# Performance work log

Measured on AMD Instinct MI355X. Metric: run time of the kernel, lower is better.

The kernel has to match this reference:

```python
import jax, jax.numpy as jnp
import numpy as np
from jax import lax

SIGMA = 0.03
ALPHA = 1.0
MASK_VALUE = -1e-8
SAMPLE_NUM = 131072  # static stand-in for the dynamic edge-pixel count


def _sobel_edges(images):
    # images: [n,3,h,w]; torch code uses only channel 0 when c==3
    kx = jnp.array([[-1., 0., 1.], [-2., 0., 2.], [-1., 0., 1.]], dtype=images.dtype).reshape(1, 1, 3, 3)
    ky = jnp.array([[1., 2., 1.], [0., 0., 0.], [-1., -2., -1.]], dtype=images.dtype).reshape(1, 1, 3, 3)
    x = images[:, :1]
    dn = ('NCHW', 'OIHW', 'NCHW')
    gx = lax.conv_general_dilated(x, kx, (1, 1), 'VALID', dimension_numbers=dn)
    gy = lax.conv_general_dilated(x, ky, (1, 1), 'VALID', dimension_numbers=dn)
    edges = jnp.sqrt(gx * gx + gy * gy)
    thetas = jnp.arctan2(gy, gx)
    pad = ((0, 0), (0, 0), (1, 1), (1, 1))
    return jnp.pad(edges, pad), jnp.pad(thetas, pad)


def _per_image_loss(inp, tgt, msk, edge, theta, ra, rd, rp, h, w):
    # all flat vectors of length P = h*w; ra:[S], rd:[4,S], rp:[2S]
    # --- edge-guided sampling ---
    emax = edge.max()
    emask = edge >= 0.1 * emax
    minlen = jnp.maximum(emask.sum(), 1)
    edge_idx = jnp.argsort(jnp.logical_not(emask), stable=True)  # edge pixels first
    anchor_pix = edge_idx[ra % minlen]
    theta_a = theta[anchor_pix]
    row_a = anchor_pix // w
    col_a = anchor_pix % w
    sign = jnp.array([-1., -1., 1., 1.], dtype=inp.dtype)[:, None]
    dist = (rd.astype(inp.dtype) + 2.0) * sign  # magnitudes in [2,31)
    col4 = jnp.clip(col_a[None, :] + jnp.round(dist * jnp.cos(theta_a)[None, :]).astype(jnp.int32), 0, w - 1)
    row4 = jnp.clip(row_a[None, :] + jnp.round(dist * jnp.sin(theta_a)[None, :]).astype(jnp.int32), 0, h - 1)
    pix = row4 * w + col4  # sub2ind, [4,S]
    A = jnp.concatenate([pix[0], pix[1], pix[2]])  # [3S]
    B = jnp.concatenate([pix[1], pix[2], pix[3]])
    # --- random sampling among valid (targets > threshold) pixels ---
    vmask = tgt > MASK_VALUE
    nvalid = jnp.maximum(vmask.sum(), 1)
    vidx = jnp.argsort(jnp.logical_not(vmask), stable=True)
    sh = rp % nvalid
    rA = vidx[sh[0::2]]
    rB = vidx[sh[1::2]]
    Ai = jnp.concatenate([A, rA])  # [4S]
    Bi = jnp.concatenate([B, rB])
    iA, iB = inp[Ai], inp[Bi]
    tA, tB = tgt[Ai], tgt[Bi]
    mA, mB = msk[Ai], msk[Bi]
    # --- ranking loss ---
    ratio = (tA + 1e-6) / (tB + 1e-6)
    hi = 1.0 + SIGMA
    lo = 1.0 / hi
    mask_eq = (ratio < hi) & (ratio > lo)
    labels = jnp.where(ratio >= hi, 1.0, 0.0) + jnp.where(ratio <= lo, -1.0, 0.0)
    cm = mA * mB
    equal_loss = (iA - iB) ** 2 * mask_eq.astype(inp.dtype) * cm
    unequal_loss = jnp.log1p(jnp.exp((iB - iA) * labels)) * (~mask_eq).astype(inp.dtype) * cm
    return ALPHA * equal_loss.mean() + unequal_loss.mean()


def reference(inputs, targets, images, rand_anchor, rand_dist, rand_perm):
    n, c, h, w = targets.shape
    masks = (targets > MASK_VALUE).astype(targets.dtype)
    edges, thetas = _sobel_edges(images)
    P = h * w
    flat = lambda x: x.reshape(n, P)
    per_img = lambda i, t, m, e, th, ra, rd, rp: _per_image_loss(i, t, m, e, th, ra, rd, rp, h, w)
    losses = jax.vmap(per_img)(flat(inputs), flat(targets), flat(masks), flat(edges), flat(thetas),
                               rand_anchor, rand_dist, rand_perm)
    return (losses.sum() / n).astype(jnp.float32)


def setup_inputs() -> dict:
    key = jax.random.key(0)
    k1, k2, k3, k4, k5, k6 = jax.random.split(key, 6)
    n, h, w = 4, 768, 1024
    P = h * w
    S = SAMPLE_NUM
    return {
        'inputs': jax.random.normal(k1, (n, 1, h, w), dtype=jnp.float32),
        'targets': jax.random.uniform(k2, (n, 1, h, w), dtype=jnp.float32),
        'images': jax.random.uniform(k3, (n, 3, h, w), dtype=jnp.float32),
        'rand_anchor': jax.random.randint(k4, (n, S), 0, P, dtype=jnp.int32),
        'rand_dist': jax.random.randint(k5, (n, 4, S), 0, 29, dtype=jnp.int32),
        'rand_perm': jax.random.randint(k6, (n, 2 * S), 0, P, dtype=jnp.int32),
    }
```

## Files before the change

### kernel.cpp

```cpp
#include <hip/hip_runtime.h>
#include <hip/hip_fp16.h>
#include <math.h>

#define W 1024
#define H 768
#define PIX (W*H)
#define NIMG 4
#define SNUM 131072
#define BPI 3072
#define NBP (NIMG*BPI)
#define UPB 12
#define NBC 1024
#define MASKV (-1e-8f)

__device__ __forceinline__ void sobel_g(const float* __restrict__ img, int y, int x,
                                        float& gx, float& gy) {
    const float* r0 = img + (y - 1) * W + x;
    const float* r1 = r0 + W;
    const float* r2 = r1 + W;
    float a00 = r0[-1], a01 = r0[0], a02 = r0[1];
    float a10 = r1[-1],              a12 = r1[1];
    float a20 = r2[-1], a21 = r2[0], a22 = r2[1];
    gx = (a02 - a00) + 2.f * (a12 - a10) + (a22 - a20);
    gy = (a00 - a20) + 2.f * (a01 - a21) + (a02 - a22);
}

__global__ void prep_kernel(const float* __restrict__ inputs,
                            const float* __restrict__ targets,
                            const float* __restrict__ images,
                            __half2* __restrict__ pairIT,
                            float* __restrict__ blockmax,
                            int* __restrict__ blkV) {
    int b = blockIdx.x, t = threadIdx.x;
    int i = b / BPI, unit = b - i * BPI;
    int gp = unit * 256 + t;
    int y = gp >> 10, x = gp & (W - 1);
    const float* img = images + (size_t)i * 3 * PIX;
    float e = 0.f;
    if (y >= 1 && y <= H - 2 && x >= 1 && x <= W - 2) {
        float gx, gy;
        sobel_g(img, y, x, gx, gy);
        e = sqrtf(gx * gx + gy * gy);
    }
    size_t off = (size_t)i * PIX + gp;
    float inv = inputs[off], tgv = targets[off];
    __half2 h;
    h.x = __float2half_rn(inv);
    h.y = __float2half_rn(tgv);
    pairIT[off] = h;

    int lane = t & 63, w = t >> 6;
    unsigned long long mV = __ballot(tgv > MASKV);
    __shared__ float sm[256];
    __shared__ int sW[4];
    if (lane == 0) sW[w] = __popcll(mV);
    sm[t] = e;
    __syncthreads();
    if (t == 0) blkV[b] = sW[0] + sW[1] + sW[2] + sW[3];
    for (int o = 128; o > 0; o >>= 1) {
        if (t < o) sm[t] = fmaxf(sm[t], sm[t + o]);
        __syncthreads();
    }
    if (t == 0) blockmax[b] = sm[0];
}

__global__ void compact_kernel(const float* __restrict__ images,
                               const float* __restrict__ targets,
                               const float* __restrict__ blockmax,
                               const int* __restrict__ blkV,
                               float2* __restrict__ anchorSeg,
                               int* __restrict__ compVSeg,
                               int* __restrict__ cntE,
                               int* __restrict__ SVg,
                               int* __restrict__ vtotG) {
    int blk = blockIdx.x, t = threadIdx.x;
    int i = blk >> 8, bb = blk & 255;
    const float* img = images + (size_t)i * 3 * PIX;
    int lane = t & 63, w = t >> 6;
    unsigned long long lm = (1ull << lane) - 1ull;

    __shared__ float sRed[256];
    __shared__ int sRedI[256];
    __shared__ int sW2[4];
    const float* bm = blockmax + i * BPI;
    const int* bv = blkV + i * BPI;
    float mx = 0.f; int sv = 0;
#pragma unroll
    for (int k = 0; k < 12; k++) { mx = fmaxf(mx, bm[t + k * 256]); sv += bv[t + k * 256]; }
    sRed[t] = mx; sRedI[t] = sv;
    __syncthreads();
    for (int o = 128; o > 0; o >>= 1) {
        if (t < o) { sRed[t] = fmaxf(sRed[t], sRed[t + o]); sRedI[t] += sRedI[t + o]; }
        __syncthreads();
    }
    float thr = 0.1f * sRed[0];
    int vtotR = sRedI[0];

    for (int k = 0; k < UPB; k++) {
        int unit = bb * UPB + k;
        int gp = unit * 256 + t;
        int y = gp >> 10, x = gp & (W - 1);
        float e = 0.f, gx = 0.f, gy = 0.f;
        bool inner = (y >= 1 && y <= H - 2 && x >= 1 && x <= W - 2);
        if (inner) { sobel_g(img, y, x, gx, gy); e = sqrtf(gx * gx + gy * gy); }
        bool isE = (e >= thr);
        unsigned long long mE = __ballot(isE);
        __syncthreads();
        if (lane == 0) sW2[w] = __popcll(mE);
        __syncthreads();
        int base = 0;
        for (int q = 0; q < w; q++) base += sW2[q];
        if (t == 0) cntE[i * BPI + unit] = sW2[0] + sW2[1] + sW2[2] + sW2[3];
        if (isE) {
            float th = inner ? atan2f(gy, gx) : 0.f;
            anchorSeg[(size_t)i * PIX + unit * 256 + base + __popcll(mE & lm)] =
                make_float2(__int_as_float(gp), th);
        }
    }

    if (vtotR < PIX) {
        for (int k = 0; k < UPB; k++) {
            int unit = bb * UPB + k;
            int gp = unit * 256 + t;
            bool v = targets[(size_t)i * PIX + gp] > MASKV;
            unsigned long long mV = __ballot(v);
            __syncthreads();
            if (lane == 0) sW2[w] = __popcll(mV);
            __syncthreads();
            int base = 0;
            for (int q = 0; q < w; q++) base += sW2[q];
            if (v) compVSeg[(size_t)i * PIX + unit * 256 + base + __popcll(mV & lm)] = gp;
        }
    }

    if (bb == 0) {
        __syncthreads();
        __shared__ int sT[256];
        int loc[12]; int tot = 0;
#pragma unroll
        for (int k = 0; k < 12; k++) { loc[k] = bv[t * 12 + k]; tot += loc[k]; }
        sT[t] = tot;
        __syncthreads();
        for (int o = 1; o < 256; o <<= 1) {
            int v = (t >= o) ? sT[t - o] : 0;
            __syncthreads();
            sT[t] += v;
            __syncthreads();
        }
        int run = sT[t] - tot;
        int* svp = SVg + i * BPI;
#pragma unroll
        for (int k = 0; k < 12; k++) { svp[t * 12 + k] = run; run += loc[k]; }
        if (t == 255) vtotG[i] = sT[255];
    }
}

__device__ __forceinline__ void pair_term(float2 a, float2 b, float& eqs, float& uns) {
    float cm = ((a.y > MASKV) ? 1.f : 0.f) * ((b.y > MASKV) ? 1.f : 0.f);
    float ratio = (a.y + 1e-6f) / (b.y + 1e-6f);
    const float HIv = 1.03f;
    const float LOv = (float)(1.0 / 1.03);
    bool eq = (ratio < HIv) && (ratio > LOv);
    if (eq) {
        float d = a.x - b.x;
        eqs += d * d * cm;
    } else {
        float label = ((ratio >= HIv) ? 1.f : 0.f) + ((ratio <= LOv) ? -1.f : 0.f);
        uns += log1pf(expf((b.x - a.x) * label)) * cm;
    }
}

__device__ __forceinline__ float2 h2f(__half2 h) {
    return make_float2(__half2float(h.x), __half2float(h.y));
}

__global__ void loss_kernel(const __half2* __restrict__ pairIT,
                            const float2* __restrict__ anchorSeg,
                            const int* __restrict__ compVSeg,
                            const int* __restrict__ cntE,
                            const int* __restrict__ SVg,
                            const int* __restrict__ vtotG,
                            const int* __restrict__ ra, const int* __restrict__ rd,
                            const int* __restrict__ rp,
                            float2* __restrict__ partials) {
    int b = blockIdx.x, t = threadIdx.x;
    int i = b & 3;
    int sub = b >> 2;
    __shared__ int S[BPI];
    __shared__ int sT[256];
    {
        const int* ce = cntE + i * BPI;
        int loc[12]; int tot = 0;
#pragma unroll
        for (int k = 0; k < 12; k++) { loc[k] = ce[t * 12 + k]; tot += loc[k]; }
        sT[t] = tot;
        __syncthreads();
        for (int o = 1; o < 256; o <<= 1) {
            int v = (t >= o) ? sT[t - o] : 0;
            __syncthreads();
            sT[t] += v;
            __syncthreads();
        }
        int run = sT[t] - tot;
#pragma unroll
        for (int k = 0; k < 12; k++) { S[t * 12 + k] = run; run += loc[k]; }
        __syncthreads();
    }
    int eT = sT[255];
    int vT = vtotG[i];
    int nval = (vT > 0) ? vT : 1;

    int s = sub * 256 + t;
    const __half2* pIT = pairIT + (size_t)i * PIX;

    int j = ra[(size_t)i * SNUM + s] % eT;
    int lo = 0, hi = BPI - 1;
#pragma unroll
    for (int k = 0; k < 12; k++) {
        int mid = (lo + hi + 1) >> 1;
        if (S[mid] <= j) lo = mid; else hi = mid - 1;
    }
    float2 ac = anchorSeg[(size_t)i * PIX + lo * 256 + (j - S[lo])];
    int anchor = __float_as_int(ac.x);
    float sv = sinf(ac.y), cv = cosf(ac.y);
    int row_a = anchor >> 10, col_a = anchor & (W - 1);

    int pix4[4];
#pragma unroll
    for (int k = 0; k < 4; k++) {
        int r = rd[((size_t)i * 4 + k) * SNUM + s];
        float dist = ((float)r + 2.0f) * ((k < 2) ? -1.f : 1.f);
        int cc = col_a + (int)rintf(dist * cv);
        int rr = row_a + (int)rintf(dist * sv);
        cc = min(max(cc, 0), W - 1);
        rr = min(max(rr, 0), H - 1);
        pix4[k] = (rr << 10) | cc;
    }
    int2 rr2 = *(const int2*)(rp + (size_t)i * 2 * SNUM + 2 * s);
    int r0 = rr2.x % nval, r1 = rr2.y % nval;
    int A, B;
    if ((vT == PIX) || (vT == 0)) {
        A = r0; B = r1;
    } else {
        const int* SV = SVg + i * BPI;
        int lo2 = 0, hi2 = BPI - 1;
        int lo3 = 0, hi3 = BPI - 1;
#pragma unroll
        for (int k = 0; k < 12; k++) {
            int m2 = (lo2 + hi2 + 1) >> 1;
            if (SV[m2] <= r0) lo2 = m2; else hi2 = m2 - 1;
            int m3 = (lo3 + hi3 + 1) >> 1;
            if (SV[m3] <= r1) lo3 = m3; else hi3 = m3 - 1;
        }
        A = compVSeg[(size_t)i * PIX + lo2 * 256 + (r0 - SV[lo2])];
        B = compVSeg[(size_t)i * PIX + lo3 * 256 + (r1 - SV[lo3])];
    }

    float2 a0 = h2f(pIT[pix4[0]]), a1 = h2f(pIT[pix4[1]]);
    float2 a2 = h2f(pIT[pix4[2]]), a3 = h2f(pIT[pix4[3]]);
    float2 b0 = h2f(pIT[A]), b1 = h2f(pIT[B]);
    float eqs = 0.f, uns = 0.f;
    pair_term(a0, a1, eqs, uns);
    pair_term(a1, a2, eqs, uns);
    pair_term(a2, a3, eqs, uns);
    pair_term(b0, b1, eqs, uns);

    __shared__ float sEq[256], sUn[256];
    sEq[t] = eqs; sUn[t] = uns;
    __syncthreads();
    for (int o = 128; o > 0; o >>= 1) {
        if (t < o) { sEq[t] += sEq[t + o]; sUn[t] += sUn[t + o]; }
        __syncthreads();
    }
    if (t == 0)
        partials[b] = make_float2(sEq[0], sUn[0]);
}

__global__ void final_kernel(const float2* __restrict__ partials, float* __restrict__ out) {
    int t = threadIdx.x;
    double acc = 0.0;
#pragma unroll
    for (int k = 0; k < 8; k++) {
        float2 p = partials[t + k * 256];
        acc += (double)p.x + (double)p.y;
    }
    __shared__ double sm[256];
    sm[t] = acc;
    __syncthreads();
    for (int o = 128; o > 0; o >>= 1) {
        if (t < o) sm[t] += sm[t + o];
        __syncthreads();
    }
    if (t == 0) {
        double denom = 4.0 * (double)SNUM;
        out[0] = (float)(sm[0] / denom / (double)NIMG);
    }
}

extern "C" void kernel_launch(void* const* d_in, const int* in_sizes, int n_in,
                              void* d_out, int out_size, void* d_ws, size_t ws_size,
                              hipStream_t stream) {
    const float* inputs  = (const float*)d_in[0];
    const float* targets = (const float*)d_in[1];
    const float* images  = (const float*)d_in[2];
    const int* ra = (const int*)d_in[3];
    const int* rd = (const int*)d_in[4];
    const int* rp = (const int*)d_in[5];
    float* out = (float*)d_out;

    char* ws = (char*)d_ws;
    int*      vtotG    = (int*)ws;
    float*    blockmax = (float*)(ws + 1024);
    int*      blkV     = (int*)(ws + 50176);
    int*      cntE     = (int*)(ws + 99328);
    int*      SVg      = (int*)(ws + 148480);
    float2*   partials = (float2*)(ws + 197632);
    __half2*  pairIT   = (__half2*)(ws + 1048576);
    float2*   anchorSeg= (float2*)(ws + 14680064);
    int*      compVSeg = (int*)(ws + 39845888);

    prep_kernel<<<NBP, 256, 0, stream>>>(inputs, targets, images,
                                         pairIT, blockmax, blkV);
    compact_kernel<<<NBC, 256, 0, stream>>>(images, targets, blockmax, blkV,
                                            anchorSeg, compVSeg, cntE, SVg, vtotG);
    loss_kernel<<<2048, 256, 0, stream>>>(pairIT, anchorSeg, compVSeg,
                                          cntE, SVg, vtotG,
                                          ra, rd, rp, partials);
    final_kernel<<<1, 256, 0, stream>>>(partials, out);
}
```

Before: 164.0 us.

## Coarsen compaction segments to 3072 pixels and shrink prefix-search tables

Changes the granularity of per-block statistics and compaction segments from 256-pixel units to 3072-pixel segments. prep_kernel now processes 12 units per block with wave-shuffle reductions, and the loss kernel's prefix scan and binary search run over 256 entries instead of 3072, which shrinks shared memory and search depth. The compact kernel drops one barrier per iteration with double-buffered counters, and the loss kernel uses __sincosf and shuffle reductions. The risks are the reduced accuracy of __sincosf, which can move rounded offsets, and fewer, larger blocks in prep.

```diff
diff --git a/kernel.cpp b/kernel.cpp
--- a/kernel.cpp
+++ b/kernel.cpp
@@ -7,10 +7,9 @@
 #define PIX (W*H)
 #define NIMG 4
 #define SNUM 131072
-#define BPI 3072
-#define NBP (NIMG*BPI)
-#define UPB 12
-#define NBC 1024
+#define SEG 3072
+#define NSEG 256
+#define NBLK (NIMG*NSEG)
 #define MASKV (-1e-8f)
 
 __device__ __forceinline__ void sobel_g(const float* __restrict__ img, int y, int x,
@@ -25,133 +24,123 @@
     gy = (a00 - a20) + 2.f * (a01 - a21) + (a02 - a22);
 }
 
-__global__ void prep_kernel(const float* __restrict__ inputs,
-                            const float* __restrict__ targets,
-                            const float* __restrict__ images,
-                            __half2* __restrict__ pairIT,
-                            float* __restrict__ blockmax,
-                            int* __restrict__ blkV) {
+__global__ __launch_bounds__(256) void prep_kernel(const float* __restrict__ inputs,
+                                                   const float* __restrict__ targets,
+                                                   const float* __restrict__ images,
+                                                   __half2* __restrict__ pairIT,
+                                                   float* __restrict__ blockmaxB,
+                                                   int* __restrict__ blkVB) {
     int b = blockIdx.x, t = threadIdx.x;
-    int i = b / BPI, unit = b - i * BPI;
-    int gp = unit * 256 + t;
-    int y = gp >> 10, x = gp & (W - 1);
+    int i = b >> 8, bb = b & 255;
     const float* img = images + (size_t)i * 3 * PIX;
-    float e = 0.f;
-    if (y >= 1 && y <= H - 2 && x >= 1 && x <= W - 2) {
-        float gx, gy;
-        sobel_g(img, y, x, gx, gy);
-        e = sqrtf(gx * gx + gy * gy);
-    }
-    size_t off = (size_t)i * PIX + gp;
-    float inv = inputs[off], tgv = targets[off];
-    __half2 h;
-    h.x = __float2half_rn(inv);
-    h.y = __float2half_rn(tgv);
-    pairIT[off] = h;
-
+    const float* inp = inputs + (size_t)i * PIX;
+    const float* tgt = targets + (size_t)i * PIX;
+    __half2* pIT = pairIT + (size_t)i * PIX;
+
+    float mx = 0.f; int vc = 0;
+#pragma unroll
+    for (int k = 0; k < 12; k++) {
+        int gp = bb * SEG + k * 256 + t;
+        int y = gp >> 10, x = gp & (W - 1);
+        float e = 0.f;
+        if (y >= 1 && y <= H - 2 && x >= 1 && x <= W - 2) {
+            float gx, gy;
+            sobel_g(img, y, x, gx, gy);
+            e = sqrtf(gx * gx + gy * gy);
+        }
+        mx = fmaxf(mx, e);
+        float inv = inp[gp], tgv = tgt[gp];
+        __half2 h;
+        h.x = __float2half_rn(inv);
+        h.y = __float2half_rn(tgv);
+        pIT[gp] = h;
+        vc += (tgv > MASKV) ? 1 : 0;
+    }
+    for (int o = 32; o; o >>= 1) {
+        mx = fmaxf(mx, __shfl_down(mx, o));
+        vc += __shfl_down(vc, o);
+    }
+    __shared__ float sm[4];
+    __shared__ int sv[4];
     int lane = t & 63, w = t >> 6;
-    unsigned long long mV = __ballot(tgv > MASKV);
-    __shared__ float sm[256];
-    __shared__ int sW[4];
-    if (lane == 0) sW[w] = __popcll(mV);
-    sm[t] = e;
-    __syncthreads();
-    if (t == 0) blkV[b] = sW[0] + sW[1] + sW[2] + sW[3];
-    for (int o = 128; o > 0; o >>= 1) {
-        if (t < o) sm[t] = fmaxf(sm[t], sm[t + o]);
-        __syncthreads();
-    }
-    if (t == 0) blockmax[b] = sm[0];
-}
-
-__global__ void compact_kernel(const float* __restrict__ images,
-                               const float* __restrict__ targets,
-                               const float* __restrict__ blockmax,
-                               const int* __restrict__ blkV,
-                               float2* __restrict__ anchorSeg,
-                               int* __restrict__ compVSeg,
-                               int* __restrict__ cntE,
-                               int* __restrict__ SVg,
-                               int* __restrict__ vtotG) {
-    int blk = blockIdx.x, t = threadIdx.x;
-    int i = blk >> 8, bb = blk & 255;
-    const float* img = images + (size_t)i * 3 * PIX;
+    if (lane == 0) { sm[w] = mx; sv[w] = vc; }
+    __syncthreads();
+    if (t == 0) {
+        blockmaxB[b] = fmaxf(fmaxf(sm[0], sm[1]), fmaxf(sm[2], sm[3]));
+        blkVB[b] = sv[0] + sv[1] + sv[2] + sv[3];
+    }
+}
+
+__global__ __launch_bounds__(256) void compact_kernel(const float* __restrict__ images,
+                                                      const float* __restrict__ targets,
+                                                      const float* __restrict__ blockmaxB,
+                                                      const int* __restrict__ blkVB,
+                                                      float2* __restrict__ anchorSeg,
+                                                      int* __restrict__ compVSeg,
+                                                      int* __restrict__ cntEB,
+                                                      int* __restrict__ cntVB,
+                                                      int* __restrict__ vtotG) {
+    int b = blockIdx.x, t = threadIdx.x;
+    int i = b >> 8, bb = b & 255;
     int lane = t & 63, w = t >> 6;
     unsigned long long lm = (1ull << lane) - 1ull;
-
-    __shared__ float sRed[256];
-    __shared__ int sRedI[256];
-    __shared__ int sW2[4];
-    const float* bm = blockmax + i * BPI;
-    const int* bv = blkV + i * BPI;
-    float mx = 0.f; int sv = 0;
-#pragma unroll
-    for (int k = 0; k < 12; k++) { mx = fmaxf(mx, bm[t + k * 256]); sv += bv[t + k * 256]; }
-    sRed[t] = mx; sRedI[t] = sv;
-    __syncthreads();
-    for (int o = 128; o > 0; o >>= 1) {
-        if (t < o) { sRed[t] = fmaxf(sRed[t], sRed[t + o]); sRedI[t] += sRedI[t + o]; }
-        __syncthreads();
-    }
-    float thr = 0.1f * sRed[0];
-    int vtotR = sRedI[0];
-
-    for (int k = 0; k < UPB; k++) {
-        int unit = bb * UPB + k;
-        int gp = unit * 256 + t;
+    const float* img = images + (size_t)i * 3 * PIX;
+
+    __shared__ float sR[256];
+    __shared__ int sI[256];
+    sR[t] = blockmaxB[(i << 8) + t];
+    sI[t] = blkVB[(i << 8) + t];
+    __syncthreads();
+    for (int o = 128; o; o >>= 1) {
+        if (t < o) { sR[t] = fmaxf(sR[t], sR[t + o]); sI[t] += sI[t + o]; }
+        __syncthreads();
+    }
+    float thr = 0.1f * sR[0];
+    int vtot = sI[0];
+    if (bb == 0 && t == 0) vtotG[i] = vtot;
+
+    __shared__ int sW2[2][4];
+    int baseE = 0;
+    float2* aSeg = anchorSeg + (size_t)i * PIX + (size_t)bb * SEG;
+    for (int k = 0; k < 12; k++) {
+        int gp = bb * SEG + k * 256 + t;
         int y = gp >> 10, x = gp & (W - 1);
         float e = 0.f, gx = 0.f, gy = 0.f;
         bool inner = (y >= 1 && y <= H - 2 && x >= 1 && x <= W - 2);
         if (inner) { sobel_g(img, y, x, gx, gy); e = sqrtf(gx * gx + gy * gy); }
         bool isE = (e >= thr);
         unsigned long long mE = __ballot(isE);
-        __syncthreads();
-        if (lane == 0) sW2[w] = __popcll(mE);
-        __syncthreads();
-        int base = 0;
-        for (int q = 0; q < w; q++) base += sW2[q];
-        if (t == 0) cntE[i * BPI + unit] = sW2[0] + sW2[1] + sW2[2] + sW2[3];
+        int* sw = sW2[k & 1];
+        if (lane == 0) sw[w] = __popcll(mE);
+        __syncthreads();
+        int base = baseE;
+        for (int q = 0; q < w; q++) base += sw[q];
         if (isE) {
             float th = inner ? atan2f(gy, gx) : 0.f;
-            anchorSeg[(size_t)i * PIX + unit * 256 + base + __popcll(mE & lm)] =
-                make_float2(__int_as_float(gp), th);
-        }
-    }
-
-    if (vtotR < PIX) {
-        for (int k = 0; k < UPB; k++) {
-            int unit = bb * UPB + k;
-            int gp = unit * 256 + t;
-            bool v = targets[(size_t)i * PIX + gp] > MASKV;
+            aSeg[base + __popcll(mE & lm)] = make_float2(__int_as_float(gp), th);
+        }
+        baseE += sw[0] + sw[1] + sw[2] + sw[3];
+    }
+    if (t == 0) cntEB[(i << 8) + bb] = baseE;
+
+    if (vtot < PIX) {
+        const float* tgt = targets + (size_t)i * PIX;
+        int* vSeg = compVSeg + (size_t)i * PIX + (size_t)bb * SEG;
+        int baseV = 0;
+        for (int k = 0; k < 12; k++) {
+            int gp = bb * SEG + k * 256 + t;
+            bool v = tgt[gp] > MASKV;
             unsigned long long mV = __ballot(v);
+            int* sw = sW2[k & 1];
+            if (k == 0) __syncthreads();
+            if (lane == 0) sw[w] = __popcll(mV);
             __syncthreads();
-            if (lane == 0) sW2[w] = __popcll(mV);
-            __syncthreads();
-            int base = 0;
-            for (int q = 0; q < w; q++) base += sW2[q];
-            if (v) compVSeg[(size_t)i * PIX + unit * 256 + base + __popcll(mV & lm)] = gp;
-        }
-    }
-
-    if (bb == 0) {
-        __syncthreads();
-        __shared__ int sT[256];
-        int loc[12]; int tot = 0;
-#pragma unroll
-        for (int k = 0; k < 12; k++) { loc[k] = bv[t * 12 + k]; tot += loc[k]; }
-        sT[t] = tot;
-        __syncthreads();
-        for (int o = 1; o < 256; o <<= 1) {
-            int v = (t >= o) ? sT[t - o] : 0;
-            __syncthreads();
-            sT[t] += v;
-            __syncthreads();
-        }
-        int run = sT[t] - tot;
-        int* svp = SVg + i * BPI;
-#pragma unroll
-        for (int k = 0; k < 12; k++) { svp[t * 12 + k] = run; run += loc[k]; }
-        if (t == 255) vtotG[i] = sT[255];
+            int base = baseV;
+            for (int q = 0; q < w; q++) base += sw[q];
+            if (v) vSeg[base + __popcll(mV & lm)] = gp;
+            baseV += sw[0] + sw[1] + sw[2] + sw[3];
+        }
+        if (t == 0) cntVB[(i << 8) + bb] = baseV;
     }
 }
 
@@ -174,26 +163,43 @@
     return make_float2(__half2float(h.x), __half2float(h.y));
 }
 
-__global__ void loss_kernel(const __half2* __restrict__ pairIT,
-                            const float2* __restrict__ anchorSeg,
-                            const int* __restrict__ compVSeg,
-                            const int* __restrict__ cntE,
-                            const int* __restrict__ SVg,
-                            const int* __restrict__ vtotG,
-                            const int* __restrict__ ra, const int* __restrict__ rd,
-                            const int* __restrict__ rp,
-                            float2* __restrict__ partials) {
+__global__ __launch_bounds__(256) void loss_kernel(const __half2* __restrict__ pairIT,
+                                                   const float2* __restrict__ anchorSeg,
+                                                   const int* __restrict__ compVSeg,
+                                                   const int* __restrict__ cntEB,
+                                                   const int* __restrict__ cntVB,
+                                                   const int* __restrict__ vtotG,
+                                                   const int* __restrict__ ra,
+                                                   const int* __restrict__ rd,
+                                                   const int* __restrict__ rp,
+                                                   float2* __restrict__ partials) {
     int b = blockIdx.x, t = threadIdx.x;
     int i = b & 3;
     int sub = b >> 2;
-    __shared__ int S[BPI];
+
     __shared__ int sT[256];
-    {
-        const int* ce = cntE + i * BPI;
-        int loc[12]; int tot = 0;
-#pragma unroll
-        for (int k = 0; k < 12; k++) { loc[k] = ce[t * 12 + k]; tot += loc[k]; }
-        sT[t] = tot;
+    __shared__ int SE[256];
+    __shared__ int SV[256];
+    __shared__ int sTot[1];
+
+    int c = cntEB[(i << 8) + t];
+    sT[t] = c;
+    __syncthreads();
+    for (int o = 1; o < 256; o <<= 1) {
+        int v = (t >= o) ? sT[t - o] : 0;
+        __syncthreads();
+        sT[t] += v;
+        __syncthreads();
+    }
+    SE[t] = sT[t] - c;
+    if (t == 255) sTot[0] = sT[255];
+    __syncthreads();
+    int eT = sTot[0];
+    int vT = vtotG[i];
+    bool needV = (vT > 0) && (vT < PIX);
+    if (needV) {
+        int cv = cntVB[(i << 8) + t];
+        sT[t] = cv;
         __syncthreads();
         for (int o = 1; o < 256; o <<= 1) {
             int v = (t >= o) ? sT[t - o] : 0;
@@ -201,28 +207,25 @@
             sT[t] += v;
             __syncthreads();
         }
-        int run = sT[t] - tot;
-#pragma unroll
-        for (int k = 0; k < 12; k++) { S[t * 12 + k] = run; run += loc[k]; }
-        __syncthreads();
-    }
-    int eT = sT[255];
-    int vT = vtotG[i];
+        SV[t] = sT[t] - cv;
+        __syncthreads();
+    }
     int nval = (vT > 0) ? vT : 1;
 
     int s = sub * 256 + t;
     const __half2* pIT = pairIT + (size_t)i * PIX;
 
     int j = ra[(size_t)i * SNUM + s] % eT;
-    int lo = 0, hi = BPI - 1;
-#pragma unroll
-    for (int k = 0; k < 12; k++) {
-        int mid = (lo + hi + 1) >> 1;
-        if (S[mid] <= j) lo = mid; else hi = mid - 1;
-    }
-    float2 ac = anchorSeg[(size_t)i * PIX + lo * 256 + (j - S[lo])];
+    int lo = 0;
+#pragma unroll
+    for (int st = 128; st; st >>= 1) {
+        int n = lo + st;
+        if (SE[n] <= j) lo = n;
+    }
+    float2 ac = anchorSeg[(size_t)i * PIX + (size_t)lo * SEG + (j - SE[lo])];
     int anchor = __float_as_int(ac.x);
-    float sv = sinf(ac.y), cv = cosf(ac.y);
+    float sv, cv;
+    __sincosf(ac.y, &sv, &cv);
     int row_a = anchor >> 10, col_a = anchor & (W - 1);
 
     int pix4[4];
@@ -239,21 +242,19 @@
     int2 rr2 = *(const int2*)(rp + (size_t)i * 2 * SNUM + 2 * s);
     int r0 = rr2.x % nval, r1 = rr2.y % nval;
     int A, B;
-    if ((vT == PIX) || (vT == 0)) {
+    if (!needV) {
         A = r0; B = r1;
     } else {
-        const int* SV = SVg + i * BPI;
-        int lo2 = 0, hi2 = BPI - 1;
-        int lo3 = 0, hi3 = BPI - 1;
-#pragma unroll
-        for (int k = 0; k < 12; k++) {
-            int m2 = (lo2 + hi2 + 1) >> 1;
-            if (SV[m2] <= r0) lo2 = m2; else hi2 = m2 - 1;
-            int m3 = (lo3 + hi3 + 1) >> 1;
-            if (SV[m3] <= r1) lo3 = m3; else hi3 = m3 - 1;
-        }
-        A = compVSeg[(size_t)i * PIX + lo2 * 256 + (r0 - SV[lo2])];
-        B = compVSeg[(size_t)i * PIX + lo3 * 256 + (r1 - SV[lo3])];
+        int lo2 = 0, lo3 = 0;
+#pragma unroll
+        for (int st = 128; st; st >>= 1) {
+            int n2 = lo2 + st;
+            if (SV[n2] <= r0) lo2 = n2;
+            int n3 = lo3 + st;
+            if (SV[n3] <= r1) lo3 = n3;
+        }
+        A = compVSeg[(size_t)i * PIX + (size_t)lo2 * SEG + (r0 - SV[lo2])];
+        B = compVSeg[(size_t)i * PIX + (size_t)lo3 * SEG + (r1 - SV[lo3])];
     }
 
     float2 a0 = h2f(pIT[pix4[0]]), a1 = h2f(pIT[pix4[1]]);
@@ -265,18 +266,21 @@
     pair_term(a2, a3, eqs, uns);
     pair_term(b0, b1, eqs, uns);
 
-    __shared__ float sEq[256], sUn[256];
-    sEq[t] = eqs; sUn[t] = uns;
-    __syncthreads();
-    for (int o = 128; o > 0; o >>= 1) {
-        if (t < o) { sEq[t] += sEq[t + o]; sUn[t] += sUn[t + o]; }
-        __syncthreads();
-    }
+    for (int o = 32; o; o >>= 1) {
+        eqs += __shfl_down(eqs, o);
+        uns += __shfl_down(uns, o);
+    }
+    __shared__ float sE4[4], sU4[4];
+    int lane = t & 63, w = t >> 6;
+    if (lane == 0) { sE4[w] = eqs; sU4[w] = uns; }
+    __syncthreads();
     if (t == 0)
-        partials[b] = make_float2(sEq[0], sUn[0]);
-}
-
-__global__ void final_kernel(const float2* __restrict__ partials, float* __restrict__ out) {
+        partials[b] = make_float2(sE4[0] + sE4[1] + sE4[2] + sE4[3],
+                                  sU4[0] + sU4[1] + sU4[2] + sU4[3]);
+}
+
+__global__ __launch_bounds__(256) void final_kernel(const float2* __restrict__ partials,
+                                                    float* __restrict__ out) {
     int t = threadIdx.x;
     double acc = 0.0;
 #pragma unroll
@@ -309,22 +313,22 @@
     float* out = (float*)d_out;
 
     char* ws = (char*)d_ws;
-    int*      vtotG    = (int*)ws;
-    float*    blockmax = (float*)(ws + 1024);
-    int*      blkV     = (int*)(ws + 50176);
-    int*      cntE     = (int*)(ws + 99328);
-    int*      SVg      = (int*)(ws + 148480);
-    float2*   partials = (float2*)(ws + 197632);
-    __half2*  pairIT   = (__half2*)(ws + 1048576);
-    float2*   anchorSeg= (float2*)(ws + 14680064);
-    int*      compVSeg = (int*)(ws + 39845888);
-
-    prep_kernel<<<NBP, 256, 0, stream>>>(inputs, targets, images,
-                                         pairIT, blockmax, blkV);
-    compact_kernel<<<NBC, 256, 0, stream>>>(images, targets, blockmax, blkV,
-                                            anchorSeg, compVSeg, cntE, SVg, vtotG);
+    int*      vtotG     = (int*)ws;
+    float*    blockmaxB = (float*)(ws + 1024);
+    int*      blkVB     = (int*)(ws + 8192);
+    int*      cntEB     = (int*)(ws + 16384);
+    int*      cntVB     = (int*)(ws + 24576);
+    float2*   partials  = (float2*)(ws + 32768);
+    __half2*  pairIT    = (__half2*)(ws + 1048576);
+    float2*   anchorSeg = (float2*)(ws + 14680064);
+    int*      compVSeg  = (int*)(ws + 39845888);
+
+    prep_kernel<<<NBLK, 256, 0, stream>>>(inputs, targets, images,
+                                          pairIT, blockmaxB, blkVB);
+    compact_kernel<<<NBLK, 256, 0, stream>>>(images, targets, blockmaxB, blkVB,
+                                             anchorSeg, compVSeg, cntEB, cntVB, vtotG);
     loss_kernel<<<2048, 256, 0, stream>>>(pairIT, anchorSeg, compVSeg,
-                                          cntE, SVg, vtotG,
+                                          cntEB, cntVB, vtotG,
                                           ra, rd, rp, partials);
     final_kernel<<<1, 256, 0, stream>>>(partials, out);
 }
```

Measured after the change: 168.3 us. 1.03x slower.
